# Kernel tuning notes

Hardware: AMD Instinct MI355X
Metric: run time of the kernel (lower is better)

## Reference

```python
import jax, jax.numpy as jnp
import numpy as np

N, E, D = 100000, 1600000, 128

def setup_inputs() -> dict:
    key = jax.random.key(0)
    ks = jax.random.split(key, 8)
    s = 1.0 / np.sqrt(D)
    return {
        "x": jax.random.normal(ks[0], (N, D), dtype=jnp.float32),
        "edge_index": jax.random.randint(ks[1], (2, E), 0, N, dtype=jnp.int64),
        "Wl0": jax.random.uniform(ks[2], (D, D), jnp.float32, -s, s),
        "Wr0": jax.random.uniform(ks[3], (D, D), jnp.float32, -s, s),
        "b0": jnp.zeros((D,), jnp.float32),
        "Wl1": jax.random.uniform(ks[4], (D, D), jnp.float32, -s, s),
        "Wr1": jax.random.uniform(ks[5], (D, D), jnp.float32, -s, s),
        "b1": jnp.zeros((D,), jnp.float32),
    }

def reference(x, edge_index, Wl0, Wr0, b0, Wl1, Wr1, b1):
    # SAGEConv (mean aggr, root_weight=True): out = mean_{j in N(i)} h_j @ Wl + h_i @ Wr + b
    src, dst = edge_index[0], edge_index[1]
    n = x.shape[0]
    # in-degree counts for mean aggregation (clamped to avoid div-by-zero)
    cnt = jax.ops.segment_sum(jnp.ones((src.shape[0],), x.dtype), dst, num_segments=n)
    denom = jnp.maximum(cnt, 1.0)[:, None]  # [N,1]

    def sage_layer(h, Wl, Wr, b):
        agg = jax.ops.segment_sum(h[src], dst, num_segments=n) / denom  # [N,D]
        # norm='none', dropout inactive at inference -> just relu
        return jax.nn.relu(agg @ Wl + h @ Wr + b)

    h = sage_layer(x, Wl0, Wr0, b0)
    h = sage_layer(h, Wl1, Wr1, b1)
    return h
```

## Files before the change

kernel.cpp:

```cpp
#include <hip/hip_runtime.h>
#include <hip/hip_bf16.h>


#define D 128
#define WSTRIDE 136
#define WPANEL (D * WSTRIDE)
#define GCAP 12288
#define BPB 8192

typedef __attribute__((ext_vector_type(8))) short short8v;
typedef __attribute__((ext_vector_type(4))) float f32x4;

__device__ inline unsigned short f2bf(float f) {
  unsigned u = __float_as_uint(f);
  return (unsigned short)((u + 0x7FFFu + ((u >> 16) & 1u)) >> 16);
}
__device__ inline unsigned pack2(float lo, float hi) {
  return (unsigned)f2bf(lo) | ((unsigned)f2bf(hi) << 16);
}

__device__ inline void dot2lo(unsigned u, float& a) {
  asm("v_dot2_f32_bf16 %0, %1, %2, %0" : "+v"(a) : "v"(u), "s"(0x00003F80u));
}
__device__ inline void dot2hi(unsigned u, float& a) {
  asm("v_dot2_f32_bf16 %0, %1, 1.0, %0" : "+v"(a) : "v"(u));
}


__global__ __launch_bounds__(256) void k_bin(const int* __restrict__ ei, int E,
                                             int* __restrict__ gcur,
                                             int* __restrict__ gbuf) {
  __shared__ int hcnt[256], hbase[256], hfill[256];
  int tid = threadIdx.x;
  hcnt[tid] = 0;
  __syncthreads();
  int e0 = blockIdx.x * BPB;
#pragma unroll
  for (int it = 0; it < BPB / 256; ++it) {
    int e = e0 + it * 256 + tid;
    if (e < E) atomicAdd(&hcnt[ei[E + e] >> 9], 1);
  }
  __syncthreads();
  int c = hcnt[tid];
  hbase[tid] = c ? atomicAdd(&gcur[tid], c) : 0;
  hfill[tid] = 0;
  __syncthreads();
#pragma unroll
  for (int it = 0; it < BPB / 256; ++it) {
    int e = e0 + it * 256 + tid;
    if (e < E) {
      int s = ei[e], d = ei[E + e];
      int bk = d >> 9;
      int slot = atomicAdd(&hfill[bk], 1);
      gbuf[(size_t)bk * GCAP + hbase[bk] + slot] = (s << 9) | (d & 511);
    }
  }
}


__global__ __launch_bounds__(256) void k_hist(const int* __restrict__ gcur,
                                              const int* __restrict__ gbuf,
                                              int* __restrict__ cnt, int n) {
  __shared__ int hc[512];
  int b = blockIdx.x, tid = threadIdx.x;
  hc[tid] = 0; hc[tid + 256] = 0;
  __syncthreads();
  int m = gcur[b];
  for (int i = tid; i < m; i += 256)
    atomicAdd(&hc[gbuf[(size_t)b * GCAP + i] & 511], 1);
  __syncthreads();
#pragma unroll
  for (int k = 0; k < 2; ++k) {
    int i = k * 256 + tid, node = b * 512 + i;
    if (node < n) cnt[node] = hc[i];
  }
}


__global__ __launch_bounds__(1024) void k_scan1(const int* __restrict__ cnt, int n,
                                                int* __restrict__ rowptr,
                                                float* __restrict__ inv_denom,
                                                int* __restrict__ bsum) {
  __shared__ int wsum[16];
  int tid = threadIdx.x, lane = tid & 63, wid = tid >> 6;
  int i = blockIdx.x * 1024 + tid;
  int v = (i < n) ? cnt[i] : 0;
  int x = v;
#pragma unroll
  for (int off = 1; off < 64; off <<= 1) {
    int t = __shfl_up(x, (unsigned)off);
    if (lane >= off) x += t;
  }
  if (lane == 63) wsum[wid] = x;
  __syncthreads();
  if (tid < 16) {
    int w = wsum[tid], y = w;
#pragma unroll
    for (int off = 1; off < 16; off <<= 1) {
      int t = __shfl_up(y, (unsigned)off);
      if (tid >= off) y += t;
    }
    wsum[tid] = y - w;
  }
  __syncthreads();
  if (i < n) {
    rowptr[i] = wsum[wid] + x - v;
    inv_denom[i] = 1.0f / (float)((v > 1) ? v : 1);
  }
  if (tid == 1023) bsum[blockIdx.x] = wsum[15] + x;
}

__global__ __launch_bounds__(64) void k_scan2(int* __restrict__ bsum, int nb,
                                              int* __restrict__ rowptr, int n) {
  int lane = threadIdx.x;
  int v0 = (lane < nb) ? bsum[lane] : 0;
  int v1 = (64 + lane < nb) ? bsum[64 + lane] : 0;
  int x = v0;
#pragma unroll
  for (int off = 1; off < 64; off <<= 1) {
    int t = __shfl_up(x, (unsigned)off);
    if (lane >= off) x += t;
  }
  int tot0 = __shfl(x, 63);
  int y = v1;
#pragma unroll
  for (int off = 1; off < 64; off <<= 1) {
    int t = __shfl_up(y, (unsigned)off);
    if (lane >= off) y += t;
  }
  if (lane < nb) bsum[lane] = x - v0;
  if (64 + lane < nb) bsum[64 + lane] = tot0 + (y - v1);
  if (lane == 63) rowptr[n] = tot0 + y;
}

__global__ __launch_bounds__(1024) void k_scan3(int* __restrict__ rowptr,
                                                const int* __restrict__ bsum, int n) {
  int i = blockIdx.x * 1024 + threadIdx.x;
  if (i < n) rowptr[i] += bsum[blockIdx.x];
}


__global__ __launch_bounds__(256) void k_place(const int* __restrict__ gcur,
                                               const int* __restrict__ gbuf,
                                               const int* __restrict__ rowptr,
                                               int* __restrict__ csr, int n) {
  __shared__ int rp[512], hf[512];
  int b = blockIdx.x, tid = threadIdx.x;
#pragma unroll
  for (int k = 0; k < 2; ++k) {
    int i = k * 256 + tid, node = b * 512 + i;
    rp[i] = (node < n) ? rowptr[node] : 0;
    hf[i] = 0;
  }
  __syncthreads();
  int m = gcur[b];
  for (int i = tid; i < m; i += 256) {
    int ent = gbuf[(size_t)b * GCAP + i];
    int d = ent & 511, s = ent >> 9;
    csr[rp[d] + atomicAdd(&hf[d], 1)] = s;
  }
}


__global__ __launch_bounds__(256) void k_tobf16(const float* __restrict__ in,
                                                short* __restrict__ ob, long long ng) {
  long long i = (long long)blockIdx.x * 256 + threadIdx.x;
  if (i >= ng) return;
  const float4* p = (const float4*)in + i * 2;
  float4 a = p[0], b = p[1];
  uint4 o;
  o.x = pack2(a.x, a.y); o.y = pack2(a.z, a.w);
  o.z = pack2(b.x, b.y); o.w = pack2(b.z, b.w);
  ((uint4*)ob)[i] = o;
}


__global__ __launch_bounds__(256) void k_wprep_frag(const float* __restrict__ W0,
                                                    const float* __restrict__ W1,
                                                    const float* __restrict__ W2,
                                                    const float* __restrict__ W3,
                                                    short* __restrict__ WF) {
  const float* W = (blockIdx.y == 0) ? W0 : (blockIdx.y == 1) ? W1
                 : (blockIdx.y == 2) ? W2 : W3;
  short* o = WF + (size_t)blockIdx.y * (D * D);
  int i = blockIdx.x * 256 + threadIdx.x;
  if (i < D * D) {
    int j = i & 7, l = (i >> 3) & 63, cc = (i >> 9) & 7, t = i >> 12;
    int k = t * 32 + (l >> 4) * 8 + j;
    int c = cc * 16 + (l & 15);
    o[i] = (short)f2bf(W[k * D + c]);
  }
}


__global__ __launch_bounds__(256) void k_wprep(const float* __restrict__ W0,
                                               const float* __restrict__ W1,
                                               const float* __restrict__ W2,
                                               const float* __restrict__ W3,
                                               short* __restrict__ WT) {
  const float* W = (blockIdx.y == 0) ? W0 : (blockIdx.y == 1) ? W1
                 : (blockIdx.y == 2) ? W2 : W3;
  short* o = WT + (size_t)blockIdx.y * WPANEL;
  int i = blockIdx.x * 256 + threadIdx.x;
  if (i < D * D) {
    int k = i >> 7, c = i & 127;
    o[c * WSTRIDE + k] = (short)f2bf(W[i]);
  }
}


__global__ __launch_bounds__(256) void k_agg_bf(const short* __restrict__ hb,
                                                const int* __restrict__ rowptr,
                                                const int* __restrict__ csr,
                                                const float* __restrict__ inv_denom,
                                                short* __restrict__ agg, int n) {
  int gw = (int)((blockIdx.x * 256u + threadIdx.x) >> 6);
  if (gw >= n) return;
  int lane = threadIdx.x & 63;
  int q = lane >> 4, s16 = lane & 15;
  int beg = __builtin_amdgcn_readfirstlane(rowptr[gw]);
  int end = __builtin_amdgcn_readfirstlane(rowptr[gw + 1]);
  float a0 = 0.f, a1 = 0.f, a2 = 0.f, a3 = 0.f;
  float a4 = 0.f, a5 = 0.f, a6 = 0.f, a7 = 0.f;
  auto addrow = [&](uint4 v) {
    dot2lo(v.x, a0); dot2hi(v.x, a1);
    dot2lo(v.y, a2); dot2hi(v.y, a3);
    dot2lo(v.z, a4); dot2hi(v.z, a5);
    dot2lo(v.w, a6); dot2hi(v.w, a7);
  };
  int e = beg + q;
  for (; e + 12 < end; e += 16) {
    int s0 = csr[e], s1 = csr[e + 4], s2 = csr[e + 8], s3 = csr[e + 12];
    uint4 v0 = ((const uint4*)(hb + (size_t)s0 * D))[s16];
    uint4 v1 = ((const uint4*)(hb + (size_t)s1 * D))[s16];
    uint4 v2 = ((const uint4*)(hb + (size_t)s2 * D))[s16];
    uint4 v3 = ((const uint4*)(hb + (size_t)s3 * D))[s16];
    addrow(v0); addrow(v1); addrow(v2); addrow(v3);
  }
  for (; e + 4 < end; e += 8) {
    int s0 = csr[e], s1 = csr[e + 4];
    uint4 v0 = ((const uint4*)(hb + (size_t)s0 * D))[s16];
    uint4 v1 = ((const uint4*)(hb + (size_t)s1 * D))[s16];
    addrow(v0); addrow(v1);
  }
  if (e < end) {
    int s0 = csr[e];
    uint4 v0 = ((const uint4*)(hb + (size_t)s0 * D))[s16];
    addrow(v0);
  }
  a0 += __shfl_xor(a0, 16); a0 += __shfl_xor(a0, 32);
  a1 += __shfl_xor(a1, 16); a1 += __shfl_xor(a1, 32);
  a2 += __shfl_xor(a2, 16); a2 += __shfl_xor(a2, 32);
  a3 += __shfl_xor(a3, 16); a3 += __shfl_xor(a3, 32);
  a4 += __shfl_xor(a4, 16); a4 += __shfl_xor(a4, 32);
  a5 += __shfl_xor(a5, 16); a5 += __shfl_xor(a5, 32);
  a6 += __shfl_xor(a6, 16); a6 += __shfl_xor(a6, 32);
  a7 += __shfl_xor(a7, 16); a7 += __shfl_xor(a7, 32);
  if (q == 0) {
    float iv = inv_denom[gw];
    uint4 o;
    o.x = pack2(a0 * iv, a1 * iv);
    o.y = pack2(a2 * iv, a3 * iv);
    o.z = pack2(a4 * iv, a5 * iv);
    o.w = pack2(a6 * iv, a7 * iv);
    ((uint4*)(agg + (size_t)gw * D))[s16] = o;
  }
}


template <int OUTF>
__global__ __launch_bounds__(256) void k_fgemm_bf(const short* __restrict__ A,
                                                  const short* __restrict__ H,
                                                  const short* __restrict__ WFl,
                                                  const short* __restrict__ WFr,
                                                  const float* __restrict__ bias,
                                                  void* __restrict__ outv, int n) {
  int tid = threadIdx.x;
  int lane = tid & 63, w4 = tid >> 6;
  int nt = (n + 31) >> 5;
  int wtile = blockIdx.x * 4 + w4;
  if (wtile >= nt) return;
  int c = lane & 15, g = lane >> 4;
  int r0 = wtile * 32;
  int row0 = r0 + c, row1 = r0 + 16 + c;
  bool ok0 = row0 < n, ok1 = row1 < n;

  float bv[8];
#pragma unroll
  for (int cc = 0; cc < 8; ++cc) bv[cc] = bias[cc * 16 + c];

  const short8v* Fl = (const short8v*)WFl;
  const short8v* Fr = (const short8v*)WFr;

  f32x4 acc0[8], acc1[8];
#pragma unroll
  for (int cc = 0; cc < 8; ++cc) {
    acc0[cc] = (f32x4){0.f, 0.f, 0.f, 0.f};
    acc1[cc] = (f32x4){0.f, 0.f, 0.f, 0.f};
  }

#pragma unroll
  for (int t = 0; t < 4; ++t) {
    short8v a0 = (short8v){0,0,0,0,0,0,0,0}, h0 = a0, a1 = a0, h1 = a0;
    int kb = t * 32 + g * 8;
    if (ok0) {
      a0 = *(const short8v*)(A + (size_t)row0 * D + kb);
      h0 = *(const short8v*)(H + (size_t)row0 * D + kb);
    }
    if (ok1) {
      a1 = *(const short8v*)(A + (size_t)row1 * D + kb);
      h1 = *(const short8v*)(H + (size_t)row1 * D + kb);
    }
#pragma unroll
    for (int cc = 0; cc < 8; ++cc) {
      short8v bl = Fl[(t * 8 + cc) * 64 + lane];
      short8v br = Fr[(t * 8 + cc) * 64 + lane];
      acc0[cc] = __builtin_amdgcn_mfma_f32_16x16x32_bf16(a0, bl, acc0[cc], 0, 0, 0);
      acc0[cc] = __builtin_amdgcn_mfma_f32_16x16x32_bf16(h0, br, acc0[cc], 0, 0, 0);
      acc1[cc] = __builtin_amdgcn_mfma_f32_16x16x32_bf16(a1, bl, acc1[cc], 0, 0, 0);
      acc1[cc] = __builtin_amdgcn_mfma_f32_16x16x32_bf16(h1, br, acc1[cc], 0, 0, 0);
    }
  }

#pragma unroll
  for (int cc = 0; cc < 8; ++cc) {
#pragma unroll
    for (int i = 0; i < 4; ++i) {
      int rr0 = r0 + g * 4 + i;
      int rr1 = rr0 + 16;
      float o0 = acc0[cc][i] + bv[cc];
      float o1 = acc1[cc][i] + bv[cc];
      o0 = o0 > 0.f ? o0 : 0.f;
      o1 = o1 > 0.f ? o1 : 0.f;
      if (OUTF) {
        if (rr0 < n) ((float*)outv)[(size_t)rr0 * D + cc * 16 + c] = o0;
        if (rr1 < n) ((float*)outv)[(size_t)rr1 * D + cc * 16 + c] = o1;
      } else {
        if (rr0 < n) ((short*)outv)[(size_t)rr0 * D + cc * 16 + c] = (short)f2bf(o0);
        if (rr1 < n) ((short*)outv)[(size_t)rr1 * D + cc * 16 + c] = (short)f2bf(o1);
      }
    }
  }
}


__global__ __launch_bounds__(256) void k_agg_f32(const float* __restrict__ h,
                                                 const int* __restrict__ rowptr,
                                                 const int* __restrict__ csr,
                                                 const float* __restrict__ inv_denom,
                                                 float* __restrict__ agg, int n) {
  int gw = (int)((blockIdx.x * 256u + threadIdx.x) >> 6);
  if (gw >= n) return;
  int lane = threadIdx.x & 63;
  int half = lane >> 5, sub = lane & 31;
  int beg = __builtin_amdgcn_readfirstlane(rowptr[gw]);
  int end = __builtin_amdgcn_readfirstlane(rowptr[gw + 1]);
  float sx0 = 0.f, sy0 = 0.f, sz0 = 0.f, sw0 = 0.f;
  float sx1 = 0.f, sy1 = 0.f, sz1 = 0.f, sw1 = 0.f;
  int e = beg;
  for (; e + 4 <= end; e += 4) {
    int i0 = csr[e + half];
    int i1 = csr[e + 2 + half];
    float4 v0 = ((const float4*)(h + (size_t)i0 * D))[sub];
    float4 v1 = ((const float4*)(h + (size_t)i1 * D))[sub];
    sx0 += v0.x; sy0 += v0.y; sz0 += v0.z; sw0 += v0.w;
    sx1 += v1.x; sy1 += v1.y; sz1 += v1.z; sw1 += v1.w;
  }
  if (e + 2 <= end) {
    int i0 = csr[e + half];
    float4 v0 = ((const float4*)(h + (size_t)i0 * D))[sub];
    sx0 += v0.x; sy0 += v0.y; sz0 += v0.z; sw0 += v0.w;
    e += 2;
  }
  if (e < end) {
    int i0 = csr[e];
    float4 v0 = ((const float4*)(h + (size_t)i0 * D))[sub];
    if (half == 0) { sx0 += v0.x; sy0 += v0.y; sz0 += v0.z; sw0 += v0.w; }
  }
  float sx = sx0 + sx1, sy = sy0 + sy1, sz = sz0 + sz1, sw = sw0 + sw1;
  sx += __shfl_xor(sx, 32); sy += __shfl_xor(sy, 32);
  sz += __shfl_xor(sz, 32); sw += __shfl_xor(sw, 32);
  if (half == 0) {
    float iv = inv_denom[gw];
    float4 r; r.x = sx * iv; r.y = sy * iv; r.z = sz * iv; r.w = sw * iv;
    ((float4*)(agg + (size_t)gw * D))[sub] = r;
  }
}

__global__ __launch_bounds__(512) void k_fgemm_f32(const float* A, const float* H,
                                                   const short* __restrict__ WTl,
                                                   const short* __restrict__ WTr,
                                                   const float* __restrict__ bias,
                                                   float* out, int n) {
  __shared__ short wl[WPANEL];
  __shared__ short wr[WPANEL];
  int tid = threadIdx.x;
  for (int i = tid; i < WPANEL / 8; i += 512) {
    ((int4*)wl)[i] = ((const int4*)WTl)[i];
    ((int4*)wr)[i] = ((const int4*)WTr)[i];
  }
  __syncthreads();
  int lane = tid & 63, wid = tid >> 6;
  int c = lane & 15, g = lane >> 4;
  float bv[8];
#pragma unroll
  for (int cc = 0; cc < 8; ++cc) bv[cc] = bias[cc * 16 + c];
  int ntile = (n + 15) >> 4;
  for (int tile = blockIdx.x * 8 + wid; tile < ntile; tile += gridDim.x * 8) {
    int r0 = tile * 16;
    int row = r0 + c;
    bool rok = row < n;
    f32x4 acc[8];
#pragma unroll
    for (int cc = 0; cc < 8; ++cc) acc[cc] = (f32x4){0.f, 0.f, 0.f, 0.f};
#pragma unroll
    for (int t = 0; t < 4; ++t) {
      short8v af = (short8v){0,0,0,0,0,0,0,0};
      short8v hf = (short8v){0,0,0,0,0,0,0,0};
      if (rok) {
        const float4* pa = (const float4*)(A + (size_t)row * D + t * 32 + g * 8);
        float4 a0 = pa[0], a1 = pa[1];
        const float4* ph = (const float4*)(H + (size_t)row * D + t * 32 + g * 8);
        float4 h0 = ph[0], h1 = ph[1];
        af[0] = (short)f2bf(a0.x); af[1] = (short)f2bf(a0.y); af[2] = (short)f2bf(a0.z); af[3] = (short)f2bf(a0.w);
        af[4] = (short)f2bf(a1.x); af[5] = (short)f2bf(a1.y); af[6] = (short)f2bf(a1.z); af[7] = (short)f2bf(a1.w);
        hf[0] = (short)f2bf(h0.x); hf[1] = (short)f2bf(h0.y); hf[2] = (short)f2bf(h0.z); hf[3] = (short)f2bf(h0.w);
        hf[4] = (short)f2bf(h1.x); hf[5] = (short)f2bf(h1.y); hf[6] = (short)f2bf(h1.z); hf[7] = (short)f2bf(h1.w);
      }
      int kb = t * 32 + g * 8;
#pragma unroll
      for (int cc = 0; cc < 8; ++cc) {
        short8v bl = *(const short8v*)&wl[(cc * 16 + c) * WSTRIDE + kb];
        acc[cc] = __builtin_amdgcn_mfma_f32_16x16x32_bf16(af, bl, acc[cc], 0, 0, 0);
        short8v br = *(const short8v*)&wr[(cc * 16 + c) * WSTRIDE + kb];
        acc[cc] = __builtin_amdgcn_mfma_f32_16x16x32_bf16(hf, br, acc[cc], 0, 0, 0);
      }
    }
#pragma unroll
    for (int cc = 0; cc < 8; ++cc) {
#pragma unroll
      for (int i = 0; i < 4; ++i) {
        int rr = r0 + g * 4 + i;
        if (rr < n) {
          float o = acc[cc][i] + bv[cc];
          out[(size_t)rr * D + cc * 16 + c] = o > 0.f ? o : 0.f;
        }
      }
    }
  }
}


extern "C" void kernel_launch(void* const* d_in, const int* in_sizes, int n_in,
                              void* d_out, int out_size, void* d_ws, size_t ws_size,
                              hipStream_t stream) {
  const float* x   = (const float*)d_in[0];
  const int*   ei  = (const int*)d_in[1];
  const float* Wl0 = (const float*)d_in[2];
  const float* Wr0 = (const float*)d_in[3];
  const float* b0  = (const float*)d_in[4];
  const float* Wl1 = (const float*)d_in[5];
  const float* Wr1 = (const float*)d_in[6];
  const float* b1  = (const float*)d_in[7];
  const int N = in_sizes[0] / D;
  const int E = in_sizes[1] / 2;
  float* out = (float*)d_out;

  size_t NP = ((size_t)N + 64) & ~(size_t)63;
  size_t EP = ((size_t)E + 63) & ~(size_t)63;
  const int NBUCK = (N + 511) >> 9;

  int* W = (int*)d_ws;
  size_t off = 0;
  int*   rowptr = W + off; off += NP;
  int*   cnt    = W + off; off += NP;
  float* inv    = (float*)(W + off); off += NP;
  int*   bsum   = W + off; off += 1024;
  int*   gcur   = W + off; off += 256;
  int*   csr    = W + off; off += EP;
  short* wt     = (short*)(W + off); off += (size_t)4 * WPANEL / 2;
  short* wf     = (short*)(W + off); off += (size_t)4 * (D * D) / 2;
  size_t base = off;
  short* aggb = (short*)(W + off); off += NP * 64;
  short* xb   = (short*)(W + off); off += NP * 64;
  short* h1b  = (short*)(W + off); off += NP * 64;
  size_t need_new = off * 4;
  float* aggf = (float*)(W + base);
  bool use_bf = ws_size >= need_new;
  int* gbuf = use_bf ? (int*)xb : (int*)aggf;

  hipMemsetAsync(gcur, 0, 256 * sizeof(int), stream);

  int NB = (N + 1023) / 1024;
  k_bin<<<(E + BPB - 1) / BPB, 256, 0, stream>>>(ei, E, gcur, gbuf);
  k_hist<<<NBUCK, 256, 0, stream>>>(gcur, gbuf, cnt, N);
  k_scan1<<<NB, 1024, 0, stream>>>(cnt, N, rowptr, inv, bsum);
  k_scan2<<<1, 64, 0, stream>>>(bsum, NB, rowptr, N);
  k_scan3<<<NB, 1024, 0, stream>>>(rowptr, bsum, N);
  k_place<<<NBUCK, 256, 0, stream>>>(gcur, gbuf, rowptr, csr, N);

  int agrid = (N + 3) / 4;
  dim3 wgrid((D * D + 255) / 256, 4);

  if (use_bf) {
    k_wprep_frag<<<wgrid, 256, 0, stream>>>(Wl0, Wr0, Wl1, Wr1, wf);
    long long ng = (long long)N * (D / 8);
    k_tobf16<<<(int)((ng + 255) / 256), 256, 0, stream>>>(x, xb, ng);
    int nt32 = (N + 31) >> 5;
    int ggrid = (nt32 + 3) / 4;
    k_agg_bf<<<agrid, 256, 0, stream>>>(xb, rowptr, csr, inv, aggb, N);
    k_fgemm_bf<0><<<ggrid, 256, 0, stream>>>(aggb, xb, wf, wf + D * D, b0, h1b, N);
    k_agg_bf<<<agrid, 256, 0, stream>>>(h1b, rowptr, csr, inv, aggb, N);
    k_fgemm_bf<1><<<ggrid, 256, 0, stream>>>(aggb, h1b, wf + 2 * D * D, wf + 3 * D * D, b1, out, N);
  } else {
    k_wprep<<<wgrid, 256, 0, stream>>>(Wl0, Wr0, Wl1, Wr1, wt);
    k_agg_f32<<<agrid, 256, 0, stream>>>(x, rowptr, csr, inv, aggf, N);
    k_fgemm_f32<<<512, 512, 0, stream>>>(aggf, x, wt, wt + WPANEL, b0, out, N);
    k_agg_f32<<<agrid, 256, 0, stream>>>(out, rowptr, csr, inv, aggf, N);
    k_fgemm_f32<<<512, 512, 0, stream>>>(aggf, out, wt + 2 * WPANEL, wt + 3 * WPANEL, b1, out, N);
  }
}
```

Before: 263.7 us.

## Fuse neighbor aggregation into the SAGE GEMM via swizzled LDS tile

Merges the bf16 gather-aggregation kernel and the MFMA GEMM into one kernel per layer. Each block aggregates 128 nodes into a 32KB XOR-swizzled shared-memory tile, then runs the MFMA GEMM directly from LDS. This removes the global write and re-read of the aggregated bf16 matrix and two kernel launches. In exchange, occupancy drops because of 32KB LDS per block and far fewer blocks, and the gather phase and the GEMM phase no longer overlap within a block.

Measured after the change: 427.2 us. 1.62x slower.

```diff
diff --git a/kernel.cpp b/kernel.cpp
--- a/kernel.cpp
+++ b/kernel.cpp
@@ -209,80 +209,80 @@
 }
 
 
-__global__ __launch_bounds__(256) void k_agg_bf(const short* __restrict__ hb,
-                                                const int* __restrict__ rowptr,
-                                                const int* __restrict__ csr,
-                                                const float* __restrict__ inv_denom,
-                                                short* __restrict__ agg, int n) {
-  int gw = (int)((blockIdx.x * 256u + threadIdx.x) >> 6);
-  if (gw >= n) return;
-  int lane = threadIdx.x & 63;
+template <int OUTF>
+__global__ __launch_bounds__(256) void k_fused(const short* __restrict__ hb,
+                                               const int* __restrict__ rowptr,
+                                               const int* __restrict__ csr,
+                                               const float* __restrict__ inv_denom,
+                                               const short* __restrict__ WFl,
+                                               const short* __restrict__ WFr,
+                                               const float* __restrict__ bias,
+                                               void* __restrict__ outv, int n) {
+  __shared__ short abuf[128 * 128];
+  int tid = threadIdx.x;
+  int w = tid >> 6, lane = tid & 63;
   int q = lane >> 4, s16 = lane & 15;
-  int beg = __builtin_amdgcn_readfirstlane(rowptr[gw]);
-  int end = __builtin_amdgcn_readfirstlane(rowptr[gw + 1]);
-  float a0 = 0.f, a1 = 0.f, a2 = 0.f, a3 = 0.f;
-  float a4 = 0.f, a5 = 0.f, a6 = 0.f, a7 = 0.f;
-  auto addrow = [&](uint4 v) {
-    dot2lo(v.x, a0); dot2hi(v.x, a1);
-    dot2lo(v.y, a2); dot2hi(v.y, a3);
-    dot2lo(v.z, a4); dot2hi(v.z, a5);
-    dot2lo(v.w, a6); dot2hi(v.w, a7);
-  };
-  int e = beg + q;
-  for (; e + 12 < end; e += 16) {
-    int s0 = csr[e], s1 = csr[e + 4], s2 = csr[e + 8], s3 = csr[e + 12];
-    uint4 v0 = ((const uint4*)(hb + (size_t)s0 * D))[s16];
-    uint4 v1 = ((const uint4*)(hb + (size_t)s1 * D))[s16];
-    uint4 v2 = ((const uint4*)(hb + (size_t)s2 * D))[s16];
-    uint4 v3 = ((const uint4*)(hb + (size_t)s3 * D))[s16];
-    addrow(v0); addrow(v1); addrow(v2); addrow(v3);
-  }
-  for (; e + 4 < end; e += 8) {
-    int s0 = csr[e], s1 = csr[e + 4];
-    uint4 v0 = ((const uint4*)(hb + (size_t)s0 * D))[s16];
-    uint4 v1 = ((const uint4*)(hb + (size_t)s1 * D))[s16];
-    addrow(v0); addrow(v1);
-  }
-  if (e < end) {
-    int s0 = csr[e];
-    uint4 v0 = ((const uint4*)(hb + (size_t)s0 * D))[s16];
-    addrow(v0);
-  }
-  a0 += __shfl_xor(a0, 16); a0 += __shfl_xor(a0, 32);
-  a1 += __shfl_xor(a1, 16); a1 += __shfl_xor(a1, 32);
-  a2 += __shfl_xor(a2, 16); a2 += __shfl_xor(a2, 32);
-  a3 += __shfl_xor(a3, 16); a3 += __shfl_xor(a3, 32);
-  a4 += __shfl_xor(a4, 16); a4 += __shfl_xor(a4, 32);
-  a5 += __shfl_xor(a5, 16); a5 += __shfl_xor(a5, 32);
-  a6 += __shfl_xor(a6, 16); a6 += __shfl_xor(a6, 32);
-  a7 += __shfl_xor(a7, 16); a7 += __shfl_xor(a7, 32);
-  if (q == 0) {
-    float iv = inv_denom[gw];
-    uint4 o;
-    o.x = pack2(a0 * iv, a1 * iv);
-    o.y = pack2(a2 * iv, a3 * iv);
-    o.z = pack2(a4 * iv, a5 * iv);
-    o.w = pack2(a6 * iv, a7 * iv);
-    ((uint4*)(agg + (size_t)gw * D))[s16] = o;
-  }
-}
-
-
-template <int OUTF>
-__global__ __launch_bounds__(256) void k_fgemm_bf(const short* __restrict__ A,
-                                                  const short* __restrict__ H,
-                                                  const short* __restrict__ WFl,
-                                                  const short* __restrict__ WFr,
-                                                  const float* __restrict__ bias,
-                                                  void* __restrict__ outv, int n) {
-  int tid = threadIdx.x;
-  int lane = tid & 63, w4 = tid >> 6;
-  int nt = (n + 31) >> 5;
-  int wtile = blockIdx.x * 4 + w4;
-  if (wtile >= nt) return;
+  int base = blockIdx.x * 128;
+
+  for (int r = 0; r < 32; ++r) {
+    int nd = base + r * 4 + w;
+    int rl = r * 4 + w;
+    float a0 = 0.f, a1 = 0.f, a2 = 0.f, a3 = 0.f;
+    float a4 = 0.f, a5 = 0.f, a6 = 0.f, a7 = 0.f;
+    if (nd < n) {
+      int beg = __builtin_amdgcn_readfirstlane(rowptr[nd]);
+      int end = __builtin_amdgcn_readfirstlane(rowptr[nd + 1]);
+      auto addrow = [&](uint4 v) {
+        dot2lo(v.x, a0); dot2hi(v.x, a1);
+        dot2lo(v.y, a2); dot2hi(v.y, a3);
+        dot2lo(v.z, a4); dot2hi(v.z, a5);
+        dot2lo(v.w, a6); dot2hi(v.w, a7);
+      };
+      int e = beg + q;
+      for (; e + 12 < end; e += 16) {
+        int s0 = csr[e], s1 = csr[e + 4], s2 = csr[e + 8], s3 = csr[e + 12];
+        uint4 v0 = ((const uint4*)(hb + (size_t)s0 * D))[s16];
+        uint4 v1 = ((const uint4*)(hb + (size_t)s1 * D))[s16];
+        uint4 v2 = ((const uint4*)(hb + (size_t)s2 * D))[s16];
+        uint4 v3 = ((const uint4*)(hb + (size_t)s3 * D))[s16];
+        addrow(v0); addrow(v1); addrow(v2); addrow(v3);
+      }
+      for (; e + 4 < end; e += 8) {
+        int s0 = csr[e], s1 = csr[e + 4];
+        uint4 v0 = ((const uint4*)(hb + (size_t)s0 * D))[s16];
+        uint4 v1 = ((const uint4*)(hb + (size_t)s1 * D))[s16];
+        addrow(v0); addrow(v1);
+      }
+      if (e < end) {
+        int s0 = csr[e];
+        uint4 v0 = ((const uint4*)(hb + (size_t)s0 * D))[s16];
+        addrow(v0);
+      }
+      a0 += __shfl_xor(a0, 16); a0 += __shfl_xor(a0, 32);
+      a1 += __shfl_xor(a1, 16); a1 += __shfl_xor(a1, 32);
+      a2 += __shfl_xor(a2, 16); a2 += __shfl_xor(a2, 32);
+      a3 += __shfl_xor(a3, 16); a3 += __shfl_xor(a3, 32);
+      a4 += __shfl_xor(a4, 16); a4 += __shfl_xor(a4, 32);
+      a5 += __shfl_xor(a5, 16); a5 += __shfl_xor(a5, 32);
+      a6 += __shfl_xor(a6, 16); a6 += __shfl_xor(a6, 32);
+      a7 += __shfl_xor(a7, 16); a7 += __shfl_xor(a7, 32);
+    }
+    if (q == 0) {
+      float iv = (nd < n) ? inv_denom[nd] : 0.f;
+      uint4 o;
+      o.x = pack2(a0 * iv, a1 * iv);
+      o.y = pack2(a2 * iv, a3 * iv);
+      o.z = pack2(a4 * iv, a5 * iv);
+      o.w = pack2(a6 * iv, a7 * iv);
+      int byt = (s16 * 16) ^ ((rl & 7) << 4);
+      *(uint4*)((char*)&abuf[(size_t)rl * D] + byt) = o;
+    }
+  }
+  __syncthreads();
+
   int c = lane & 15, g = lane >> 4;
-  int r0 = wtile * 32;
-  int row0 = r0 + c, row1 = r0 + 16 + c;
+  int rl0 = w * 32 + c, rl1 = rl0 + 16;
+  int row0 = base + rl0, row1 = base + rl1;
   bool ok0 = row0 < n, ok1 = row1 < n;
 
   float bv[8];
@@ -301,16 +301,13 @@
 
 #pragma unroll
   for (int t = 0; t < 4; ++t) {
-    short8v a0 = (short8v){0,0,0,0,0,0,0,0}, h0 = a0, a1 = a0, h1 = a0;
     int kb = t * 32 + g * 8;
-    if (ok0) {
-      a0 = *(const short8v*)(A + (size_t)row0 * D + kb);
-      h0 = *(const short8v*)(H + (size_t)row0 * D + kb);
-    }
-    if (ok1) {
-      a1 = *(const short8v*)(A + (size_t)row1 * D + kb);
-      h1 = *(const short8v*)(H + (size_t)row1 * D + kb);
-    }
+    int byt = (kb * 2) ^ ((rl0 & 7) << 4);
+    short8v a0 = *(const short8v*)((const char*)&abuf[(size_t)rl0 * D] + byt);
+    short8v a1 = *(const short8v*)((const char*)&abuf[(size_t)rl1 * D] + byt);
+    short8v h0 = (short8v){0,0,0,0,0,0,0,0}, h1 = h0;
+    if (ok0) h0 = *(const short8v*)(hb + (size_t)row0 * D + kb);
+    if (ok1) h1 = *(const short8v*)(hb + (size_t)row1 * D + kb);
 #pragma unroll
     for (int cc = 0; cc < 8; ++cc) {
       short8v bl = Fl[(t * 8 + cc) * 64 + lane];
@@ -326,7 +323,7 @@
   for (int cc = 0; cc < 8; ++cc) {
 #pragma unroll
     for (int i = 0; i < 4; ++i) {
-      int rr0 = r0 + g * 4 + i;
+      int rr0 = base + w * 32 + g * 4 + i;
       int rr1 = rr0 + 16;
       float o0 = acc0[cc][i] + bv[cc];
       float o1 = acc1[cc][i] + bv[cc];
@@ -481,13 +478,12 @@
   short* wt     = (short*)(W + off); off += (size_t)4 * WPANEL / 2;
   short* wf     = (short*)(W + off); off += (size_t)4 * (D * D) / 2;
   size_t base = off;
-  short* aggb = (short*)(W + off); off += NP * 64;
   short* xb   = (short*)(W + off); off += NP * 64;
   short* h1b  = (short*)(W + off); off += NP * 64;
   size_t need_new = off * 4;
   float* aggf = (float*)(W + base);
   bool use_bf = ws_size >= need_new;
-  int* gbuf = use_bf ? (int*)xb : (int*)aggf;
+  int* gbuf = use_bf ? (int*)h1b : (int*)aggf;
 
   hipMemsetAsync(gcur, 0, 256 * sizeof(int), stream);
 
@@ -499,20 +495,19 @@
   k_scan3<<<NB, 1024, 0, stream>>>(rowptr, bsum, N);
   k_place<<<NBUCK, 256, 0, stream>>>(gcur, gbuf, rowptr, csr, N);
 
-  int agrid = (N + 3) / 4;
   dim3 wgrid((D * D + 255) / 256, 4);
 
   if (use_bf) {
     k_wprep_frag<<<wgrid, 256, 0, stream>>>(Wl0, Wr0, Wl1, Wr1, wf);
     long long ng = (long long)N * (D / 8);
     k_tobf16<<<(int)((ng + 255) / 256), 256, 0, stream>>>(x, xb, ng);
-    int nt32 = (N + 31) >> 5;
-    int ggrid = (nt32 + 3) / 4;
-    k_agg_bf<<<agrid, 256, 0, stream>>>(xb, rowptr, csr, inv, aggb, N);
-    k_fgemm_bf<0><<<ggrid, 256, 0, stream>>>(aggb, xb, wf, wf + D * D, b0, h1b, N);
-    k_agg_bf<<<agrid, 256, 0, stream>>>(h1b, rowptr, csr, inv, aggb, N);
-    k_fgemm_bf<1><<<ggrid, 256, 0, stream>>>(aggb, h1b, wf + 2 * D * D, wf + 3 * D * D, b1, out, N);
+    int fgrid = (N + 127) / 128;
+    k_fused<0><<<fgrid, 256, 0, stream>>>(xb, rowptr, csr, inv,
+                                          wf, wf + D * D, b0, h1b, N);
+    k_fused<1><<<fgrid, 256, 0, stream>>>(h1b, rowptr, csr, inv,
+                                          wf + 2 * D * D, wf + 3 * D * D, b1, out, N);
   } else {
+    int agrid = (N + 3) / 4;
     k_wprep<<<wgrid, 256, 0, stream>>>(Wl0, Wr0, Wl1, Wr1, wt);
     k_agg_f32<<<agrid, 256, 0, stream>>>(x, rowptr, csr, inv, aggf, N);
     k_fgemm_f32<<<512, 512, 0, stream>>>(aggf, x, wt, wt + WPANEL, b0, out, N);
```
